# Optimization experiments

Hardware: AMD Instinct MI355X
Metric: run time of the kernel (lower is better)

The kernel has to match this reference:

```python
import jax, jax.numpy as jnp
import numpy as np

B, C, H, W = 16, 256, 64, 64


def setup_inputs() -> dict:
    key = jax.random.key(0)
    kx, ky, kz, kw, kb, kg = jax.random.split(key, 6)
    x = jax.random.normal(kx, (B, C, H, W), dtype=jnp.float32)
    y = jax.random.normal(ky, (B, C, H, W), dtype=jnp.float32)
    z = jax.random.normal(kz, (B, C, H, W), dtype=jnp.float32)
    # 1x1 conv params (stored as [out_c, in_c]); gamma is a learned scalar
    # (init 0 in the module; use a nonzero value so the output exercises the path)
    conv_w = jax.random.normal(kw, (C, C), dtype=jnp.float32) / np.sqrt(C)
    conv_b = jax.random.normal(kb, (C,), dtype=jnp.float32) * 0.01
    gamma = jax.random.normal(kg, (1,), dtype=jnp.float32) * 0.1
    return {"x": x, "y": y, "z": z, "conv_w": conv_w, "conv_b": conv_b, "gamma": gamma}


def _channel_attn(q, k_src):
    # q: [B, C, N]; k_src: [B, C, H, W] -> energy [B, C, C]
    b, c, n = q.shape
    k = k_src.reshape(b, c, n)
    energy = jnp.einsum('bcn,bdn->bcd', q, k)
    # reversed-max trick: max - energy, then softmax over last dim
    energy_new = jnp.max(energy, axis=-1, keepdims=True) - energy
    return jax.nn.softmax(energy_new, axis=-1)


def reference(x, y, z, conv_w, conv_b, gamma):
    b, c, h, w = x.shape
    q = x.reshape(b, c, h * w)  # query == key1 == value
    # three attention maps share query and value; sum before the value bmm
    attn = _channel_attn(q, x) + _channel_attn(q, y) + _channel_attn(q, z)
    out = jnp.einsum('bcd,bdn->bcn', attn, q).reshape(b, c, h, w)
    # 1x1 conv == per-pixel channel mixing
    out = jnp.einsum('oc,bchw->bohw', conv_w, out) + conv_b[None, :, None, None]
    return gamma * out + x
```

## Files before the change

kernel.cpp:

```cpp
#include <hip/hip_runtime.h>
#include <hip/hip_bf16.h>


#define B_ 16
#define C_ 256
#define N_ 4096
#define KSPLIT 4
#define KCHUNK (N_ / KSPLIT)

#define MODE_BF16 0
#define MODE_F32  1

typedef __bf16 bf16_t;
typedef bf16_t bf16x8 __attribute__((ext_vector_type(8)));
typedef float  f32x4  __attribute__((ext_vector_type(4)));

#define MFMA(a, b, c) __builtin_amdgcn_mfma_f32_16x16x32_bf16(a, b, c, 0, 0, 0)

__device__ int    g_mode;
__device__ bf16_t g_in[3][(size_t)B_ * C_ * N_];
__device__ bf16_t g_qT[(size_t)B_ * N_ * C_];
__device__ bf16_t g_cw[C_ * C_];
__device__ float  g_cb[C_];
__device__ float  g_gamma;
__device__ float  g_Ep[(size_t)KSPLIT * 3 * B_ * C_ * C_];
__device__ bf16_t g_attnT[(size_t)B_ * C_ * C_];
__device__ bf16_t g_M[(size_t)B_ * C_ * C_];
__device__ bf16_t g_P[(size_t)B_ * C_ * N_];

__global__ __launch_bounds__(256) void detect_kernel(const float* __restrict__ xf)
{
  __shared__ unsigned red[256];
  const int t = threadIdx.x;
  unsigned m = 0;
  for (int i = t; i < 4096; i += 256)
    m = max(m, __float_as_uint(xf[i]) & 0x7fffffffu);
  red[t] = m;
  __syncthreads();
  for (int s = 128; s > 0; s >>= 1) {
    if (t < s) red[t] = max(red[t], red[t + s]);
    __syncthreads();
  }
  if (t == 0) g_mode = (red[0] > 0x44800000u) ? MODE_BF16 : MODE_F32;
}

__global__ __launch_bounds__(256) void convert_big(
    const void* __restrict__ y, const void* __restrict__ z)
{
  const void* src = blockIdx.y == 0 ? y : z;
  bf16_t* dst = g_in[1 + blockIdx.y];
  const size_t idx = ((size_t)blockIdx.x * 256 + threadIdx.x) * 8;
  if (g_mode == MODE_F32) {
    const float* s = (const float*)src + idx;
    float4 a = *(const float4*)s;
    float4 b = *(const float4*)(s + 4);
    bf16x8 v;
    v[0] = (bf16_t)a.x; v[1] = (bf16_t)a.y; v[2] = (bf16_t)a.z; v[3] = (bf16_t)a.w;
    v[4] = (bf16_t)b.x; v[5] = (bf16_t)b.y; v[6] = (bf16_t)b.z; v[7] = (bf16_t)b.w;
    *(bf16x8*)(dst + idx) = v;
  } else {
    *(bf16x8*)(dst + idx) = *(const bf16x8*)((const bf16_t*)src + idx);
  }
}

__global__ __launch_bounds__(256) void convert_xT(const void* __restrict__ x)
{
  __shared__ bf16_t Ts[64][72];
  const int t  = threadIdx.x;
  const int r  = t >> 3;
  const int co = (t & 7) * 8;
  const int n0 = blockIdx.x * 64;
  const int c0 = blockIdx.y * 64;
  const int b  = blockIdx.z;
  const size_t base = (size_t)b * C_ * N_;

  bf16x8 v[2];
  if (g_mode == MODE_F32) {
#pragma unroll
    for (int p = 0; p < 2; ++p) {
      const float* s = (const float*)x + base + (size_t)(c0 + r + p * 32) * N_ + n0 + co;
      float4 a = *(const float4*)s;
      float4 b4 = *(const float4*)(s + 4);
      bf16x8 w;
      w[0] = (bf16_t)a.x; w[1] = (bf16_t)a.y; w[2] = (bf16_t)a.z; w[3] = (bf16_t)a.w;
      w[4] = (bf16_t)b4.x; w[5] = (bf16_t)b4.y; w[6] = (bf16_t)b4.z; w[7] = (bf16_t)b4.w;
      v[p] = w;
    }
  } else {
#pragma unroll
    for (int p = 0; p < 2; ++p)
      v[p] = *(const bf16x8*)((const bf16_t*)x + base + (size_t)(c0 + r + p * 32) * N_ + n0 + co);
  }

#pragma unroll
  for (int p = 0; p < 2; ++p) {
    *(bf16x8*)(g_in[0] + base + (size_t)(c0 + r + p * 32) * N_ + n0 + co) = v[p];
    *(bf16x8*)(&Ts[r + p * 32][co]) = v[p];
  }
  __syncthreads();

#pragma unroll
  for (int p = 0; p < 2; ++p) {
    const int n = r + p * 32;
    bf16x8 w;
#pragma unroll
    for (int j = 0; j < 8; ++j) w[j] = Ts[co + j][n];
    *(bf16x8*)(g_qT + (size_t)b * N_ * C_ + (size_t)(n0 + n) * C_ + c0 + co) = w;
  }
}

__global__ __launch_bounds__(256) void convert_params(
    const void* __restrict__ cw, const void* __restrict__ cb,
    const void* __restrict__ gm)
{
  const int t = threadIdx.x;
  if (g_mode == MODE_F32) {
    for (int i = t * 8; i < C_ * C_; i += 256 * 8) {
      const float* s = (const float*)cw + i;
      float4 a = *(const float4*)s;
      float4 b = *(const float4*)(s + 4);
      bf16x8 v;
      v[0] = (bf16_t)a.x; v[1] = (bf16_t)a.y; v[2] = (bf16_t)a.z; v[3] = (bf16_t)a.w;
      v[4] = (bf16_t)b.x; v[5] = (bf16_t)b.y; v[6] = (bf16_t)b.z; v[7] = (bf16_t)b.w;
      *(bf16x8*)(g_cw + i) = v;
    }
    if (t < C_) g_cb[t] = ((const float*)cb)[t];
    if (t == 0) g_gamma = ((const float*)gm)[0];
  } else {
    for (int i = t * 8; i < C_ * C_; i += 256 * 8)
      *(bf16x8*)(g_cw + i) = *(const bf16x8*)((const bf16_t*)cw + i);
    if (t < C_) g_cb[t] = (float)((const bf16_t*)cb)[t];
    if (t == 0) g_gamma = (float)((const bf16_t*)gm)[0];
  }
}

__global__ __launch_bounds__(256) void energy_kernel()
{
  const int tile = blockIdx.x & 3;
  const int kc   = blockIdx.x >> 2;
  const int s    = blockIdx.y;
  const int b    = blockIdx.z;

  const bf16_t* q = g_in[0] + (size_t)b * C_ * N_;
  const bf16_t* k = g_in[s] + (size_t)b * C_ * N_;

  const int tile_m = (tile & 1) * 128;
  const int tile_d = (tile >> 1) * 128;

  __shared__ bf16_t As[128][72];
  __shared__ bf16_t Bs[128][72];

  const int tid  = threadIdx.x;
  const int w    = tid >> 6;
  const int lane = tid & 63;
  const int wm   = (w & 1) * 64;
  const int wd   = (w >> 1) * 64;
  const int lrow = lane & 15;
  const int lk   = (lane >> 4) * 8;

  const int srow = tid >> 3;
  const int soff = (tid & 7) * 8;

  f32x4 acc[4][4] = {};

  const int kbeg = kc * KCHUNK;
  for (int k0 = kbeg; k0 < kbeg + KCHUNK; k0 += 64) {
    bf16x8 av[4], bv[4];
#pragma unroll
    for (int i = 0; i < 4; ++i) {
      int r = srow + i * 32;
      av[i] = *(const bf16x8*)(q + (size_t)(tile_m + r) * N_ + k0 + soff);
      bv[i] = *(const bf16x8*)(k + (size_t)(tile_d + r) * N_ + k0 + soff);
    }
    __syncthreads();
#pragma unroll
    for (int i = 0; i < 4; ++i) {
      int r = srow + i * 32;
      *(bf16x8*)(&As[r][soff]) = av[i];
      *(bf16x8*)(&Bs[r][soff]) = bv[i];
    }
    __syncthreads();
#pragma unroll
    for (int kk = 0; kk < 64; kk += 32) {
      bf16x8 af[4], bfr[4];
#pragma unroll
      for (int i = 0; i < 4; ++i)
        af[i] = *(const bf16x8*)(&As[wm + i * 16 + lrow][kk + lk]);
#pragma unroll
      for (int j = 0; j < 4; ++j)
        bfr[j] = *(const bf16x8*)(&Bs[wd + j * 16 + lrow][kk + lk]);
#pragma unroll
      for (int i = 0; i < 4; ++i)
#pragma unroll
        for (int j = 0; j < 4; ++j)
          acc[i][j] = MFMA(af[i], bfr[j], acc[i][j]);
    }
  }

  float* Eb = g_Ep + (((size_t)kc * 3 + s) * B_ + b) * (size_t)C_ * C_;
  const int orow0 = tile_m + wm + (lane >> 4) * 4;
  const int ocol0 = tile_d + wd + (lane & 15);
#pragma unroll
  for (int i = 0; i < 4; ++i)
#pragma unroll
    for (int j = 0; j < 4; ++j)
#pragma unroll
      for (int r = 0; r < 4; ++r)
        Eb[(size_t)(orow0 + i * 16 + r) * C_ + (ocol0 + j * 16)] = acc[i][j][r];
}

__global__ __launch_bounds__(256) void softmax_kernel()
{
  const int b    = blockIdx.y;
  const int c    = blockIdx.x * 4 + (threadIdx.x >> 6);
  const int lane = threadIdx.x & 63;
  const int d0   = lane * 4;

  float a0 = 0.f, a1 = 0.f, a2 = 0.f, a3 = 0.f;
#pragma unroll
  for (int s = 0; s < 3; ++s) {
    float e0 = 0.f, e1 = 0.f, e2 = 0.f, e3 = 0.f;
#pragma unroll
    for (int kc = 0; kc < KSPLIT; ++kc) {
      const float4 ep = *(const float4*)(
          g_Ep + ((((size_t)kc * 3 + s) * B_ + b) * C_ + c) * (size_t)C_ + d0);
      e0 += ep.x; e1 += ep.y; e2 += ep.z; e3 += ep.w;
    }
    float mn = fminf(fminf(e0, e1), fminf(e2, e3));
#pragma unroll
    for (int m = 32; m > 0; m >>= 1) mn = fminf(mn, __shfl_xor(mn, m));
    const float p0 = __expf(mn - e0);
    const float p1 = __expf(mn - e1);
    const float p2 = __expf(mn - e2);
    const float p3 = __expf(mn - e3);
    float Z = p0 + p1 + p2 + p3;
#pragma unroll
    for (int m = 32; m > 0; m >>= 1) Z += __shfl_xor(Z, m);
    const float rZ = 1.0f / Z;
    a0 += p0 * rZ; a1 += p1 * rZ; a2 += p2 * rZ; a3 += p3 * rZ;
  }
  bf16_t* At = g_attnT + (size_t)b * C_ * C_;
  At[(size_t)(d0 + 0) * C_ + c] = (bf16_t)a0;
  At[(size_t)(d0 + 1) * C_ + c] = (bf16_t)a1;
  At[(size_t)(d0 + 2) * C_ + c] = (bf16_t)a2;
  At[(size_t)(d0 + 3) * C_ + c] = (bf16_t)a3;
}

__global__ __launch_bounds__(256) void mconv_kernel()
{
  const int tile = blockIdx.x;
  const int b    = blockIdx.y;
  const int tile_o = (tile & 1) * 128;
  const int tile_d = (tile >> 1) * 128;
  const int tid  = threadIdx.x;
  const int w    = tid >> 6;
  const int lane = tid & 63;
  const int wo   = (w & 1) * 64;
  const int wd   = (w >> 1) * 64;
  const int lrow = lane & 15;
  const int lk   = (lane >> 4) * 8;

  const bf16_t* At = g_attnT + (size_t)b * C_ * C_;
  f32x4 acc[4][4] = {};

  for (int c0 = 0; c0 < C_; c0 += 32) {
    bf16x8 af[4], bfr[4];
#pragma unroll
    for (int i = 0; i < 4; ++i)
      af[i] = *(const bf16x8*)(g_cw + (size_t)(tile_o + wo + i * 16 + lrow) * C_ + c0 + lk);
#pragma unroll
    for (int j = 0; j < 4; ++j)
      bfr[j] = *(const bf16x8*)(At + (size_t)(tile_d + wd + j * 16 + lrow) * C_ + c0 + lk);
#pragma unroll
    for (int i = 0; i < 4; ++i)
#pragma unroll
      for (int j = 0; j < 4; ++j)
        acc[i][j] = MFMA(af[i], bfr[j], acc[i][j]);
  }

  bf16_t* Mb = g_M + (size_t)b * C_ * C_;
  const int orow0 = tile_o + wo + (lane >> 4) * 4;
  const int ocol0 = tile_d + wd + (lane & 15);
#pragma unroll
  for (int i = 0; i < 4; ++i)
#pragma unroll
    for (int j = 0; j < 4; ++j)
#pragma unroll
      for (int r = 0; r < 4; ++r)
        Mb[(size_t)(orow0 + i * 16 + r) * C_ + (ocol0 + j * 16)] = (bf16_t)acc[i][j][r];
}

__global__ __launch_bounds__(256) void pmq_kernel()
{
  const int tile_n = blockIdx.x * 128;
  const int tile_o = blockIdx.y * 128;
  const int b      = blockIdx.z;

  const bf16_t* Mb = g_M  + (size_t)b * C_ * C_;
  const bf16_t* Qt = g_qT + (size_t)b * N_ * C_;

  __shared__ bf16_t As[128][72];
  __shared__ bf16_t Bs[128][72];

  const int tid  = threadIdx.x;
  const int w    = tid >> 6;
  const int lane = tid & 63;
  const int wo   = (w & 1) * 64;
  const int wn   = (w >> 1) * 64;
  const int lrow = lane & 15;
  const int lk   = (lane >> 4) * 8;

  const int srow = tid >> 3;
  const int soff = (tid & 7) * 8;

  f32x4 acc[4][4] = {};

  for (int d0 = 0; d0 < C_; d0 += 64) {
    bf16x8 av[4], bv[4];
#pragma unroll
    for (int i = 0; i < 4; ++i) {
      int r = srow + i * 32;
      av[i] = *(const bf16x8*)(Mb + (size_t)(tile_o + r) * C_ + d0 + soff);
      bv[i] = *(const bf16x8*)(Qt + (size_t)(tile_n + r) * C_ + d0 + soff);
    }
    __syncthreads();
#pragma unroll
    for (int i = 0; i < 4; ++i) {
      int r = srow + i * 32;
      *(bf16x8*)(&As[r][soff]) = av[i];
      *(bf16x8*)(&Bs[r][soff]) = bv[i];
    }
    __syncthreads();
#pragma unroll
    for (int kk = 0; kk < 64; kk += 32) {
      bf16x8 af[4], bfr[4];
#pragma unroll
      for (int i = 0; i < 4; ++i)
        af[i] = *(const bf16x8*)(&As[wo + i * 16 + lrow][kk + lk]);
#pragma unroll
      for (int j = 0; j < 4; ++j)
        bfr[j] = *(const bf16x8*)(&Bs[wn + j * 16 + lrow][kk + lk]);
#pragma unroll
      for (int i = 0; i < 4; ++i)
#pragma unroll
        for (int j = 0; j < 4; ++j)
          acc[i][j] = MFMA(af[i], bfr[j], acc[i][j]);
    }
  }

  bf16_t* Pb = g_P + (size_t)b * C_ * N_;
  const int orow0 = tile_o + wo + (lane >> 4) * 4;
  const int ocol0 = tile_n + wn + (lane & 15);
#pragma unroll
  for (int i = 0; i < 4; ++i)
#pragma unroll
    for (int j = 0; j < 4; ++j)
#pragma unroll
      for (int r = 0; r < 4; ++r)
        Pb[(size_t)(orow0 + i * 16 + r) * N_ + (ocol0 + j * 16)] = (bf16_t)acc[i][j][r];
}

__global__ __launch_bounds__(256) void epilogue_kernel(
    const void* __restrict__ xraw, void* __restrict__ outraw)
{
  const int row  = blockIdx.x;
  const int o    = row & (C_ - 1);
  const size_t roff = (size_t)row * N_ + (size_t)threadIdx.x * 16;

  const float g    = g_gamma;
  const float bias = g_cb[o];

  const bf16x8 p0 = *(const bf16x8*)(g_P + roff);
  const bf16x8 p1 = *(const bf16x8*)(g_P + roff + 8);
  float v[16];
#pragma unroll
  for (int k = 0; k < 8; ++k) {
    v[k]     = g * ((float)p0[k] + bias);
    v[8 + k] = g * ((float)p1[k] + bias);
  }

  if (g_mode == MODE_F32) {
    const float* xp = (const float*)xraw + roff;
    float*       op = (float*)outraw + roff;
#pragma unroll
    for (int q4 = 0; q4 < 4; ++q4) {
      float4 xv = *(const float4*)(xp + q4 * 4);
      float4 ov;
      ov.x = v[q4 * 4 + 0] + xv.x;
      ov.y = v[q4 * 4 + 1] + xv.y;
      ov.z = v[q4 * 4 + 2] + xv.z;
      ov.w = v[q4 * 4 + 3] + xv.w;
      *(float4*)(op + q4 * 4) = ov;
    }
  } else {
    const bf16_t* xp = (const bf16_t*)xraw + roff;
    bf16_t*       op = (bf16_t*)outraw + roff;
#pragma unroll
    for (int p = 0; p < 2; ++p) {
      bf16x8 xv = *(const bf16x8*)(xp + p * 8);
      bf16x8 ov;
#pragma unroll
      for (int k = 0; k < 8; ++k)
        ov[k] = (bf16_t)(v[p * 8 + k] + (float)xv[k]);
      *(bf16x8*)(op + p * 8) = ov;
    }
  }
}

extern "C" void kernel_launch(void* const* d_in, const int* in_sizes, int n_in,
                              void* d_out, int out_size, void* d_ws, size_t ws_size,
                              hipStream_t stream)
{
  const void* x  = d_in[0];
  const void* y  = d_in[1];
  const void* z  = d_in[2];
  const void* cw = d_in[3];
  const void* cb = d_in[4];
  const void* gm = d_in[5];
  (void)d_ws; (void)ws_size;

  detect_kernel   <<<1,                       256, 0, stream>>>((const float*)x);
  convert_big     <<<dim3(8192, 2),           256, 0, stream>>>(y, z);
  convert_params  <<<1,                       256, 0, stream>>>(cw, cb, gm);
  convert_xT      <<<dim3(N_ / 64, C_ / 64, B_), 256, 0, stream>>>(x);
  energy_kernel   <<<dim3(4 * KSPLIT, 3, B_), 256, 0, stream>>>();
  softmax_kernel  <<<dim3(C_ / 4, B_),        256, 0, stream>>>();
  mconv_kernel    <<<dim3(4, B_),             256, 0, stream>>>();
  pmq_kernel      <<<dim3(N_ / 128, 2, B_),   256, 0, stream>>>();
  epilogue_kernel <<<dim3(B_ * C_),           256, 0, stream>>>(x, d_out);
}
```

Measured before the change: 406.3 us.

## Fuse y/z bf16 conversion into energy GEMM loads and widen tiles

Removes the separate convert_big pass, so the energy kernel reads y and z directly in their raw format (converting fp32 to bf16 in registers) instead of from a staged bf16 copy. Each block now computes a full 256x128 energy tile with 512 threads, so the query rows are loaded once per block rather than twice. This drops a full read-plus-write pass over two large tensors. In exchange the energy kernel reads fp32 K data, which doubles its K-side load bytes, and the larger block may lower occupancy.

```diff
diff --git a/kernel.cpp b/kernel.cpp
--- a/kernel.cpp
+++ b/kernel.cpp
@@ -18,7 +18,7 @@
 #define MFMA(a, b, c) __builtin_amdgcn_mfma_f32_16x16x32_bf16(a, b, c, 0, 0, 0)
 
 __device__ int    g_mode;
-__device__ bf16_t g_in[3][(size_t)B_ * C_ * N_];
+__device__ bf16_t g_q[(size_t)B_ * C_ * N_];
 __device__ bf16_t g_qT[(size_t)B_ * N_ * C_];
 __device__ bf16_t g_cw[C_ * C_];
 __device__ float  g_cb[C_];
@@ -44,25 +44,6 @@
   if (t == 0) g_mode = (red[0] > 0x44800000u) ? MODE_BF16 : MODE_F32;
 }
 
-__global__ __launch_bounds__(256) void convert_big(
-    const void* __restrict__ y, const void* __restrict__ z)
-{
-  const void* src = blockIdx.y == 0 ? y : z;
-  bf16_t* dst = g_in[1 + blockIdx.y];
-  const size_t idx = ((size_t)blockIdx.x * 256 + threadIdx.x) * 8;
-  if (g_mode == MODE_F32) {
-    const float* s = (const float*)src + idx;
-    float4 a = *(const float4*)s;
-    float4 b = *(const float4*)(s + 4);
-    bf16x8 v;
-    v[0] = (bf16_t)a.x; v[1] = (bf16_t)a.y; v[2] = (bf16_t)a.z; v[3] = (bf16_t)a.w;
-    v[4] = (bf16_t)b.x; v[5] = (bf16_t)b.y; v[6] = (bf16_t)b.z; v[7] = (bf16_t)b.w;
-    *(bf16x8*)(dst + idx) = v;
-  } else {
-    *(bf16x8*)(dst + idx) = *(const bf16x8*)((const bf16_t*)src + idx);
-  }
-}
-
 __global__ __launch_bounds__(256) void convert_xT(const void* __restrict__ x)
 {
   __shared__ bf16_t Ts[64][72];
@@ -94,7 +75,7 @@
 
 #pragma unroll
   for (int p = 0; p < 2; ++p) {
-    *(bf16x8*)(g_in[0] + base + (size_t)(c0 + r + p * 32) * N_ + n0 + co) = v[p];
+    *(bf16x8*)(g_q + base + (size_t)(c0 + r + p * 32) * N_ + n0 + co) = v[p];
     *(bf16x8*)(&Ts[r + p * 32][co]) = v[p];
   }
   __syncthreads();
@@ -134,51 +115,73 @@
   }
 }
 
-__global__ __launch_bounds__(256) void energy_kernel()
-{
-  const int tile = blockIdx.x & 3;
-  const int kc   = blockIdx.x >> 2;
-  const int s    = blockIdx.y;
-  const int b    = blockIdx.z;
-
-  const bf16_t* q = g_in[0] + (size_t)b * C_ * N_;
-  const bf16_t* k = g_in[s] + (size_t)b * C_ * N_;
-
-  const int tile_m = (tile & 1) * 128;
-  const int tile_d = (tile >> 1) * 128;
-
-  __shared__ bf16_t As[128][72];
+__global__ __launch_bounds__(512) void energy_kernel(
+    const void* __restrict__ yraw, const void* __restrict__ zraw)
+{
+  const int dtile = blockIdx.x & 1;
+  const int kc    = blockIdx.x >> 1;
+  const int s     = blockIdx.y;
+  const int b     = blockIdx.z;
+
+  const bf16_t* q = g_q + (size_t)b * C_ * N_;
+  const int tile_d = dtile * 128;
+
+  __shared__ bf16_t As[256][72];
   __shared__ bf16_t Bs[128][72];
 
   const int tid  = threadIdx.x;
   const int w    = tid >> 6;
   const int lane = tid & 63;
-  const int wm   = (w & 1) * 64;
-  const int wd   = (w >> 1) * 64;
+  const int wm   = (w & 3) * 64;
+  const int wd   = (w >> 2) * 64;
   const int lrow = lane & 15;
   const int lk   = (lane >> 4) * 8;
 
   const int srow = tid >> 3;
   const int soff = (tid & 7) * 8;
 
+  const int mode = g_mode;
+  const bf16_t* kb16 = nullptr;
+  const float*  kf32 = nullptr;
+  if (s == 0) {
+    kb16 = g_q + (size_t)b * C_ * N_;
+  } else if (mode == MODE_BF16) {
+    kb16 = (const bf16_t*)(s == 1 ? yraw : zraw) + (size_t)b * C_ * N_;
+  } else {
+    kf32 = (const float*)(s == 1 ? yraw : zraw) + (size_t)b * C_ * N_;
+  }
+
   f32x4 acc[4][4] = {};
 
   const int kbeg = kc * KCHUNK;
   for (int k0 = kbeg; k0 < kbeg + KCHUNK; k0 += 64) {
-    bf16x8 av[4], bv[4];
-#pragma unroll
-    for (int i = 0; i < 4; ++i) {
-      int r = srow + i * 32;
-      av[i] = *(const bf16x8*)(q + (size_t)(tile_m + r) * N_ + k0 + soff);
-      bv[i] = *(const bf16x8*)(k + (size_t)(tile_d + r) * N_ + k0 + soff);
+    bf16x8 av[4], bv[2];
+#pragma unroll
+    for (int i = 0; i < 4; ++i)
+      av[i] = *(const bf16x8*)(q + (size_t)(srow + i * 64) * N_ + k0 + soff);
+    if (kf32) {
+#pragma unroll
+      for (int i = 0; i < 2; ++i) {
+        const float* sp = kf32 + (size_t)(tile_d + srow + i * 64) * N_ + k0 + soff;
+        float4 a = *(const float4*)sp;
+        float4 c = *(const float4*)(sp + 4);
+        bf16x8 v;
+        v[0] = (bf16_t)a.x; v[1] = (bf16_t)a.y; v[2] = (bf16_t)a.z; v[3] = (bf16_t)a.w;
+        v[4] = (bf16_t)c.x; v[5] = (bf16_t)c.y; v[6] = (bf16_t)c.z; v[7] = (bf16_t)c.w;
+        bv[i] = v;
+      }
+    } else {
+#pragma unroll
+      for (int i = 0; i < 2; ++i)
+        bv[i] = *(const bf16x8*)(kb16 + (size_t)(tile_d + srow + i * 64) * N_ + k0 + soff);
     }
     __syncthreads();
 #pragma unroll
-    for (int i = 0; i < 4; ++i) {
-      int r = srow + i * 32;
-      *(bf16x8*)(&As[r][soff]) = av[i];
-      *(bf16x8*)(&Bs[r][soff]) = bv[i];
-    }
+    for (int i = 0; i < 4; ++i)
+      *(bf16x8*)(&As[srow + i * 64][soff]) = av[i];
+#pragma unroll
+    for (int i = 0; i < 2; ++i)
+      *(bf16x8*)(&Bs[srow + i * 64][soff]) = bv[i];
     __syncthreads();
 #pragma unroll
     for (int kk = 0; kk < 64; kk += 32) {
@@ -198,7 +201,7 @@
   }
 
   float* Eb = g_Ep + (((size_t)kc * 3 + s) * B_ + b) * (size_t)C_ * C_;
-  const int orow0 = tile_m + wm + (lane >> 4) * 4;
+  const int orow0 = wm + (lane >> 4) * 4;
   const int ocol0 = tile_d + wd + (lane & 15);
 #pragma unroll
   for (int i = 0; i < 4; ++i)
@@ -420,10 +423,9 @@
   (void)d_ws; (void)ws_size;
 
   detect_kernel   <<<1,                       256, 0, stream>>>((const float*)x);
-  convert_big     <<<dim3(8192, 2),           256, 0, stream>>>(y, z);
   convert_params  <<<1,                       256, 0, stream>>>(cw, cb, gm);
   convert_xT      <<<dim3(N_ / 64, C_ / 64, B_), 256, 0, stream>>>(x);
-  energy_kernel   <<<dim3(4 * KSPLIT, 3, B_), 256, 0, stream>>>();
+  energy_kernel   <<<dim3(2 * KSPLIT, 3, B_), 512, 0, stream>>>(y, z);
   softmax_kernel  <<<dim3(C_ / 4, B_),        256, 0, stream>>>();
   mconv_kernel    <<<dim3(4, B_),             256, 0, stream>>>();
   pmq_kernel      <<<dim3(N_ / 128, 2, B_),   256, 0, stream>>>();
```

After: 381.3 us. -6.2%, faster.

## Fuse y/z conversion into energy GEMM loads and merge setup kernels

Applied to the files above, without the earlier changes.

Removes the separate convert_big pass that wrote bf16 copies of y and z. The energy kernel now reads the raw fp32 (or bf16) inputs directly and converts them while loading. The detect and params kernels are merged into one launch, the transpose shared buffer uses an XOR swizzle instead of padding, and mconv uses 64x64 tiles so it launches more blocks. The aim is to cut a large round trip through global memory plus launch overhead, at the cost of energy loads fetching fp32 (twice the bytes) repeated across tiles and K-splits.

```diff
diff --git a/kernel.cpp b/kernel.cpp
--- a/kernel.cpp
+++ b/kernel.cpp
@@ -18,7 +18,7 @@
 #define MFMA(a, b, c) __builtin_amdgcn_mfma_f32_16x16x32_bf16(a, b, c, 0, 0, 0)
 
 __device__ int    g_mode;
-__device__ bf16_t g_in[3][(size_t)B_ * C_ * N_];
+__device__ bf16_t g_q[(size_t)B_ * C_ * N_];
 __device__ bf16_t g_qT[(size_t)B_ * N_ * C_];
 __device__ bf16_t g_cw[C_ * C_];
 __device__ float  g_cb[C_];
@@ -28,7 +28,9 @@
 __device__ bf16_t g_M[(size_t)B_ * C_ * C_];
 __device__ bf16_t g_P[(size_t)B_ * C_ * N_];
 
-__global__ __launch_bounds__(256) void detect_kernel(const float* __restrict__ xf)
+__global__ __launch_bounds__(256) void setup_kernel(
+    const float* __restrict__ xf, const void* __restrict__ cw,
+    const void* __restrict__ cb, const void* __restrict__ gm)
 {
   __shared__ unsigned red[256];
   const int t = threadIdx.x;
@@ -41,41 +43,44 @@
     if (t < s) red[t] = max(red[t], red[t + s]);
     __syncthreads();
   }
-  if (t == 0) g_mode = (red[0] > 0x44800000u) ? MODE_BF16 : MODE_F32;
-}
-
-__global__ __launch_bounds__(256) void convert_big(
-    const void* __restrict__ y, const void* __restrict__ z)
-{
-  const void* src = blockIdx.y == 0 ? y : z;
-  bf16_t* dst = g_in[1 + blockIdx.y];
-  const size_t idx = ((size_t)blockIdx.x * 256 + threadIdx.x) * 8;
-  if (g_mode == MODE_F32) {
-    const float* s = (const float*)src + idx;
-    float4 a = *(const float4*)s;
-    float4 b = *(const float4*)(s + 4);
-    bf16x8 v;
-    v[0] = (bf16_t)a.x; v[1] = (bf16_t)a.y; v[2] = (bf16_t)a.z; v[3] = (bf16_t)a.w;
-    v[4] = (bf16_t)b.x; v[5] = (bf16_t)b.y; v[6] = (bf16_t)b.z; v[7] = (bf16_t)b.w;
-    *(bf16x8*)(dst + idx) = v;
+  const int mode = (red[0] > 0x44800000u) ? MODE_BF16 : MODE_F32;
+  if (t == 0) g_mode = mode;
+
+  if (mode == MODE_F32) {
+    for (int i = t * 8; i < C_ * C_; i += 256 * 8) {
+      const float* s = (const float*)cw + i;
+      float4 a = *(const float4*)s;
+      float4 b = *(const float4*)(s + 4);
+      bf16x8 v;
+      v[0] = (bf16_t)a.x; v[1] = (bf16_t)a.y; v[2] = (bf16_t)a.z; v[3] = (bf16_t)a.w;
+      v[4] = (bf16_t)b.x; v[5] = (bf16_t)b.y; v[6] = (bf16_t)b.z; v[7] = (bf16_t)b.w;
+      *(bf16x8*)(g_cw + i) = v;
+    }
+    if (t < C_) g_cb[t] = ((const float*)cb)[t];
+    if (t == 0) g_gamma = ((const float*)gm)[0];
   } else {
-    *(bf16x8*)(dst + idx) = *(const bf16x8*)((const bf16_t*)src + idx);
+    for (int i = t * 8; i < C_ * C_; i += 256 * 8)
+      *(bf16x8*)(g_cw + i) = *(const bf16x8*)((const bf16_t*)cw + i);
+    if (t < C_) g_cb[t] = (float)((const bf16_t*)cb)[t];
+    if (t == 0) g_gamma = (float)((const bf16_t*)gm)[0];
   }
 }
 
 __global__ __launch_bounds__(256) void convert_xT(const void* __restrict__ x)
 {
-  __shared__ bf16_t Ts[64][72];
+  __shared__ bf16_t Ts[64][64];
   const int t  = threadIdx.x;
   const int r  = t >> 3;
-  const int co = (t & 7) * 8;
+  const int nb = t & 7;
+  const int co = nb * 8;
   const int n0 = blockIdx.x * 64;
   const int c0 = blockIdx.y * 64;
   const int b  = blockIdx.z;
   const size_t base = (size_t)b * C_ * N_;
+  const int mode = g_mode;
 
   bf16x8 v[2];
-  if (g_mode == MODE_F32) {
+  if (mode == MODE_F32) {
 #pragma unroll
     for (int p = 0; p < 2; ++p) {
       const float* s = (const float*)x + base + (size_t)(c0 + r + p * 32) * N_ + n0 + co;
@@ -94,55 +99,50 @@
 
 #pragma unroll
   for (int p = 0; p < 2; ++p) {
-    *(bf16x8*)(g_in[0] + base + (size_t)(c0 + r + p * 32) * N_ + n0 + co) = v[p];
-    *(bf16x8*)(&Ts[r + p * 32][co]) = v[p];
+    const int cl = r + p * 32;
+    if (mode == MODE_F32)
+      *(bf16x8*)(g_q + base + (size_t)(c0 + cl) * N_ + n0 + co) = v[p];
+    const int swz = nb ^ ((cl >> 3) & 7);
+    *(bf16x8*)(&Ts[cl][swz * 8]) = v[p];
   }
   __syncthreads();
 
 #pragma unroll
   for (int p = 0; p < 2; ++p) {
-    const int n = r + p * 32;
+    const int nl = r + p * 32;
     bf16x8 w;
 #pragma unroll
-    for (int j = 0; j < 8; ++j) w[j] = Ts[co + j][n];
-    *(bf16x8*)(g_qT + (size_t)b * N_ * C_ + (size_t)(n0 + n) * C_ + c0 + co) = w;
-  }
-}
-
-__global__ __launch_bounds__(256) void convert_params(
-    const void* __restrict__ cw, const void* __restrict__ cb,
-    const void* __restrict__ gm)
-{
-  const int t = threadIdx.x;
-  if (g_mode == MODE_F32) {
-    for (int i = t * 8; i < C_ * C_; i += 256 * 8) {
-      const float* s = (const float*)cw + i;
-      float4 a = *(const float4*)s;
-      float4 b = *(const float4*)(s + 4);
-      bf16x8 v;
-      v[0] = (bf16_t)a.x; v[1] = (bf16_t)a.y; v[2] = (bf16_t)a.z; v[3] = (bf16_t)a.w;
-      v[4] = (bf16_t)b.x; v[5] = (bf16_t)b.y; v[6] = (bf16_t)b.z; v[7] = (bf16_t)b.w;
-      *(bf16x8*)(g_cw + i) = v;
-    }
-    if (t < C_) g_cb[t] = ((const float*)cb)[t];
-    if (t == 0) g_gamma = ((const float*)gm)[0];
-  } else {
-    for (int i = t * 8; i < C_ * C_; i += 256 * 8)
-      *(bf16x8*)(g_cw + i) = *(const bf16x8*)((const bf16_t*)cw + i);
-    if (t < C_) g_cb[t] = (float)((const bf16_t*)cb)[t];
-    if (t == 0) g_gamma = (float)((const bf16_t*)gm)[0];
-  }
-}
-
-__global__ __launch_bounds__(256) void energy_kernel()
+    for (int j = 0; j < 8; ++j) {
+      const int c = co + j;
+      const int k = (c >> 3) & 7;
+      w[j] = Ts[c][(((nl >> 3) ^ k) * 8) + (nl & 7)];
+    }
+    *(bf16x8*)(g_qT + (size_t)b * N_ * C_ + (size_t)(n0 + nl) * C_ + c0 + co) = w;
+  }
+}
+
+__global__ __launch_bounds__(256) void energy_kernel(
+    const void* __restrict__ xraw, const void* __restrict__ yraw,
+    const void* __restrict__ zraw)
 {
   const int tile = blockIdx.x & 3;
   const int kc   = blockIdx.x >> 2;
   const int s    = blockIdx.y;
   const int b    = blockIdx.z;
 
-  const bf16_t* q = g_in[0] + (size_t)b * C_ * N_;
-  const bf16_t* k = g_in[s] + (size_t)b * C_ * N_;
+  const int mode = g_mode;
+  const bf16_t* q =
+      (mode == MODE_BF16 ? (const bf16_t*)xraw : g_q) + (size_t)b * C_ * N_;
+
+  const bf16_t* kb16 = nullptr;
+  const float*  kf32 = nullptr;
+  if (s == 0) {
+    kb16 = q;
+  } else if (mode == MODE_BF16) {
+    kb16 = (const bf16_t*)(s == 1 ? yraw : zraw) + (size_t)b * C_ * N_;
+  } else {
+    kf32 = (const float*)(s == 1 ? yraw : zraw) + (size_t)b * C_ * N_;
+  }
 
   const int tile_m = (tile & 1) * 128;
   const int tile_d = (tile >> 1) * 128;
@@ -170,7 +170,25 @@
     for (int i = 0; i < 4; ++i) {
       int r = srow + i * 32;
       av[i] = *(const bf16x8*)(q + (size_t)(tile_m + r) * N_ + k0 + soff);
-      bv[i] = *(const bf16x8*)(k + (size_t)(tile_d + r) * N_ + k0 + soff);
+    }
+    if (kf32) {
+#pragma unroll
+      for (int i = 0; i < 4; ++i) {
+        int r = srow + i * 32;
+        const float* sp = kf32 + (size_t)(tile_d + r) * N_ + k0 + soff;
+        float4 a = *(const float4*)sp;
+        float4 c = *(const float4*)(sp + 4);
+        bf16x8 v;
+        v[0] = (bf16_t)a.x; v[1] = (bf16_t)a.y; v[2] = (bf16_t)a.z; v[3] = (bf16_t)a.w;
+        v[4] = (bf16_t)c.x; v[5] = (bf16_t)c.y; v[6] = (bf16_t)c.z; v[7] = (bf16_t)c.w;
+        bv[i] = v;
+      }
+    } else {
+#pragma unroll
+      for (int i = 0; i < 4; ++i) {
+        int r = srow + i * 32;
+        bv[i] = *(const bf16x8*)(kb16 + (size_t)(tile_d + r) * N_ + k0 + soff);
+      }
     }
     __syncthreads();
 #pragma unroll
@@ -250,31 +268,31 @@
 {
   const int tile = blockIdx.x;
   const int b    = blockIdx.y;
-  const int tile_o = (tile & 1) * 128;
-  const int tile_d = (tile >> 1) * 128;
+  const int tile_o = (tile & 3) * 64;
+  const int tile_d = (tile >> 2) * 64;
   const int tid  = threadIdx.x;
   const int w    = tid >> 6;
   const int lane = tid & 63;
-  const int wo   = (w & 1) * 64;
-  const int wd   = (w >> 1) * 64;
+  const int wo   = (w & 1) * 32;
+  const int wd   = (w >> 1) * 32;
   const int lrow = lane & 15;
   const int lk   = (lane >> 4) * 8;
 
   const bf16_t* At = g_attnT + (size_t)b * C_ * C_;
-  f32x4 acc[4][4] = {};
+  f32x4 acc[2][2] = {};
 
   for (int c0 = 0; c0 < C_; c0 += 32) {
-    bf16x8 af[4], bfr[4];
-#pragma unroll
-    for (int i = 0; i < 4; ++i)
+    bf16x8 af[2], bfr[2];
+#pragma unroll
+    for (int i = 0; i < 2; ++i)
       af[i] = *(const bf16x8*)(g_cw + (size_t)(tile_o + wo + i * 16 + lrow) * C_ + c0 + lk);
 #pragma unroll
-    for (int j = 0; j < 4; ++j)
+    for (int j = 0; j < 2; ++j)
       bfr[j] = *(const bf16x8*)(At + (size_t)(tile_d + wd + j * 16 + lrow) * C_ + c0 + lk);
 #pragma unroll
-    for (int i = 0; i < 4; ++i)
-#pragma unroll
-      for (int j = 0; j < 4; ++j)
+    for (int i = 0; i < 2; ++i)
+#pragma unroll
+      for (int j = 0; j < 2; ++j)
         acc[i][j] = MFMA(af[i], bfr[j], acc[i][j]);
   }
 
@@ -282,11 +300,11 @@
   const int orow0 = tile_o + wo + (lane >> 4) * 4;
   const int ocol0 = tile_d + wd + (lane & 15);
 #pragma unroll
-  for (int i = 0; i < 4; ++i)
-#pragma unroll
-    for (int j = 0; j < 4; ++j)
-#pragma unroll
-      for (int r = 0; r < 4; ++r)
+  for (int i = 0; i < 2; ++i)
+#pragma unroll
+    for (int j = 0; j < 2; ++j)
+#pragma unroll
+      for (int r = 0; r < 2 * 2; ++r)
         Mb[(size_t)(orow0 + i * 16 + r) * C_ + (ocol0 + j * 16)] = (bf16_t)acc[i][j][r];
 }
 
@@ -419,13 +437,11 @@
   const void* gm = d_in[5];
   (void)d_ws; (void)ws_size;
 
-  detect_kernel   <<<1,                       256, 0, stream>>>((const float*)x);
-  convert_big     <<<dim3(8192, 2),           256, 0, stream>>>(y, z);
-  convert_params  <<<1,                       256, 0, stream>>>(cw, cb, gm);
+  setup_kernel    <<<1,                       256, 0, stream>>>((const float*)x, cw, cb, gm);
   convert_xT      <<<dim3(N_ / 64, C_ / 64, B_), 256, 0, stream>>>(x);
-  energy_kernel   <<<dim3(4 * KSPLIT, 3, B_), 256, 0, stream>>>();
+  energy_kernel   <<<dim3(4 * KSPLIT, 3, B_), 256, 0, stream>>>(x, y, z);
   softmax_kernel  <<<dim3(C_ / 4, B_),        256, 0, stream>>>();
-  mconv_kernel    <<<dim3(4, B_),             256, 0, stream>>>();
+  mconv_kernel    <<<dim3(16, B_),            256, 0, stream>>>();
   pmq_kernel      <<<dim3(N_ / 128, 2, B_),   256, 0, stream>>>();
   epilogue_kernel <<<dim3(B_ * C_),           256, 0, stream>>>(x, d_out);
 }
```

Result: faster. 374.2 us (-7.9%).
